# Optimization experiments

Hardware: AMD Instinct MI355X
Metric: run time of the kernel (lower is better)

The kernel has to match this reference:

```python
import jax, jax.numpy as jnp
import numpy as np

B, LT, LI, DT, DI, D, H = 128, 96, 64, 1024, 2048, 1024, 4
NEG = -2.0 ** 31  # tf.pow(-2.0, 31)
EPS = 1e-3        # keras LayerNormalization default epsilon


def _mha(q_in, k_in, v_in, q_mask, k_mask, Wq, Wk, Wv, Wo):
    # tf split-heads: chunk i of axis 2 -> head i; reshape (B,L,H,d) matches.
    d = D // H
    b = q_in.shape[0]
    q = (q_in @ Wq).reshape(b, -1, H, d)
    k = (k_in @ Wk).reshape(b, -1, H, d)
    v = (v_in @ Wv).reshape(b, -1, H, d)
    scores = jnp.einsum('bqhd,bkhd->bhqk', q, k) / jnp.sqrt(jnp.float32(d))
    mask = (q_mask != 0)[:, None, :, None] & (k_mask != 0)[:, None, None, :]  # [B,1,Lq,Lk]
    scores = jnp.where(mask, scores, NEG)
    attn = jax.nn.softmax(scores, axis=-1)
    attn = jnp.where(mask, attn, 0.0)  # dropout rate is 0.0 -> identity
    out = jnp.einsum('bhqk,bkhd->bqhd', attn, v).reshape(b, -1, D)
    return out @ Wo


def _ln(x, g, b):
    m = jnp.mean(x, axis=-1, keepdims=True)
    v = jnp.var(x, axis=-1, keepdims=True)
    return (x - m) / jnp.sqrt(v + EPS) * g + b


def setup_inputs() -> dict:
    key = jax.random.key(0)
    ks = iter(jax.random.split(key, 40))
    s = 0.02
    inp = {
        'text_embedding': jax.random.normal(next(ks), (B, LT, DT), jnp.float32),
        'image_embedding': jax.random.normal(next(ks), (B, LI, DI), jnp.float32),
        'text_mask': jax.random.randint(next(ks), (B, LT), 0, 2, jnp.int32),
        'image_mask': jax.random.randint(next(ks), (B, LI), 0, 2, jnp.int32),
        'W_tp': jax.random.normal(next(ks), (DT, D), jnp.float32) * s,
        'b_tp': jnp.zeros((D,), jnp.float32),
        'W_ip': jax.random.normal(next(ks), (DI, D), jnp.float32) * s,
        'b_ip': jnp.zeros((D,), jnp.float32),
        # text cross-attn (query=image_proj, key=text_proj, value=RAW text)
        'ta_Wq': jax.random.normal(next(ks), (D, D), jnp.float32) * s,
        'ta_Wk': jax.random.normal(next(ks), (D, D), jnp.float32) * s,
        'ta_Wv': jax.random.normal(next(ks), (DT, D), jnp.float32) * s,
        'ta_Wo': jax.random.normal(next(ks), (D, D), jnp.float32) * s,
        # image cross-attn (query=text_proj, key=image_proj, value=RAW image)
        'ia_Wq': jax.random.normal(next(ks), (D, D), jnp.float32) * s,
        'ia_Wk': jax.random.normal(next(ks), (D, D), jnp.float32) * s,
        'ia_Wv': jax.random.normal(next(ks), (DI, D), jnp.float32) * s,
        'ia_Wo': jax.random.normal(next(ks), (D, D), jnp.float32) * s,
        # self-attention blocks
        'ts_Wq': jax.random.normal(next(ks), (D, D), jnp.float32) * s,
        'ts_Wk': jax.random.normal(next(ks), (D, D), jnp.float32) * s,
        'ts_Wv': jax.random.normal(next(ks), (D, D), jnp.float32) * s,
        'ts_Wo': jax.random.normal(next(ks), (D, D), jnp.float32) * s,
        'is_Wq': jax.random.normal(next(ks), (D, D), jnp.float32) * s,
        'is_Wk': jax.random.normal(next(ks), (D, D), jnp.float32) * s,
        'is_Wv': jax.random.normal(next(ks), (D, D), jnp.float32) * s,
        'is_Wo': jax.random.normal(next(ks), (D, D), jnp.float32) * s,
        # layernorm params
        'ln_ta_g': jnp.ones((D,), jnp.float32), 'ln_ta_b': jnp.zeros((D,), jnp.float32),
        'ln_ia_g': jnp.ones((D,), jnp.float32), 'ln_ia_b': jnp.zeros((D,), jnp.float32),
        'ln_ts_g': jnp.ones((D,), jnp.float32), 'ln_ts_b': jnp.zeros((D,), jnp.float32),
        'ln_is_g': jnp.ones((D,), jnp.float32), 'ln_is_b': jnp.zeros((D,), jnp.float32),
    }
    return inp


def reference(text_embedding, image_embedding, text_mask, image_mask,
              W_tp, b_tp, W_ip, b_ip,
              ta_Wq, ta_Wk, ta_Wv, ta_Wo,
              ia_Wq, ia_Wk, ia_Wv, ia_Wo,
              ts_Wq, ts_Wk, ts_Wv, ts_Wo,
              is_Wq, is_Wk, is_Wv, is_Wo,
              ln_ta_g, ln_ta_b, ln_ia_g, ln_ia_b,
              ln_ts_g, ln_ts_b, ln_is_g, ln_is_b):
    text_proj = text_embedding @ W_tp + b_tp    # [B,LT,D]
    image_proj = image_embedding @ W_ip + b_ip  # [B,LI,D]
    # cross attention (note asymmetric query/key masks, raw-value inputs)
    text_att = _mha(image_proj, text_proj, text_embedding, image_mask, text_mask,
                    ta_Wq, ta_Wk, ta_Wv, ta_Wo)   # [B,LI,D]
    image_att = _mha(text_proj, image_proj, image_embedding, text_mask, image_mask,
                     ia_Wq, ia_Wk, ia_Wv, ia_Wo)  # [B,LT,D]
    text_att = _ln(text_att, ln_ta_g, ln_ta_b)
    image_att = _ln(image_att, ln_ia_g, ln_ia_b)
    # self attention
    text_att = _mha(text_att, text_att, text_att, image_mask, image_mask,
                    ts_Wq, ts_Wk, ts_Wv, ts_Wo)
    image_att = _mha(image_att, image_att, image_att, text_mask, text_mask,
                     is_Wq, is_Wk, is_Wv, is_Wo)
    text_att = _ln(text_att, ln_ts_g, ln_ts_b)
    image_att = _ln(image_att, ln_is_g, ln_is_b)
    return (text_att, image_att)
```

## Files before the change

### kernel.cpp

```cpp
#include <hip/hip_runtime.h>

typedef __bf16 bf16_t;
typedef __attribute__((ext_vector_type(8))) __bf16 bf16x8;
typedef __attribute__((ext_vector_type(4))) __bf16 bf16x4;
typedef __attribute__((ext_vector_type(4))) float f32x4;

__device__ __forceinline__ void async_copy16(const bf16_t* g, bf16_t* l) {
    __builtin_amdgcn_global_load_lds(
        (const __attribute__((address_space(1))) void*)g,
        (__attribute__((address_space(3))) void*)l, 16, 0, 0);
}

__global__ __launch_bounds__(256) void cvt_bf16(const float* __restrict__ in,
                                                bf16_t* __restrict__ out) {
    int i = (blockIdx.x * 256 + threadIdx.x) * 4;
    float4 v = *(const float4*)(in + i);
    bf16x4 o;
    o[0] = (__bf16)v.x; o[1] = (__bf16)v.y; o[2] = (__bf16)v.z; o[3] = (__bf16)v.w;
    *(bf16x4*)(out + i) = o;
}

__global__ __launch_bounds__(256) void transpose_group(const float* __restrict__ s0,
                                                       const float* __restrict__ s1,
                                                       const float* __restrict__ s2,
                                                       bf16_t* __restrict__ dst, int K) {
    const float* in;
    if (blockIdx.z == 0) in = s0;
    else if (blockIdx.z == 1) in = s1;
    else in = s2;
    bf16_t* out = dst + (size_t)blockIdx.z * 1024 * K;
    __shared__ float tile[32][33];
    int t = threadIdx.x;
    int tx = t & 31, ty = t >> 5;
    int n0 = blockIdx.x * 32, k0 = blockIdx.y * 32;
#pragma unroll
    for (int i = 0; i < 4; i++) {
        int k = k0 + ty + i * 8;
        tile[ty + i * 8][tx] = in[(size_t)k * 1024 + n0 + tx];
    }
    __syncthreads();
#pragma unroll
    for (int i = 0; i < 4; i++) {
        int n = n0 + ty + i * 8;
        out[(size_t)n * K + k0 + tx] = (bf16_t)tile[tx][ty + i * 8];
    }
}

__global__ __launch_bounds__(256) void fuse_bias(const float* __restrict__ src,
                                                 float* __restrict__ out) {
    int i = blockIdx.x * 256 + threadIdx.x;
    out[i] = (i < 1024) ? src[i] : 0.f;
}

__global__ __launch_bounds__(256, 2) void gemm256(const bf16_t* __restrict__ A,
                                                  const bf16_t* __restrict__ Bt,
                                                  const float* __restrict__ bias,
                                                  bf16_t* __restrict__ o0,
                                                  bf16_t* __restrict__ o1,
                                                  bf16_t* __restrict__ o2,
                                                  int M, int N, int K) {
    (void)M; (void)N;
    __shared__ bf16_t Ls[36864];
    const int t = threadIdx.x;
    const int w = t >> 6, lane = t & 63;
    const int l16 = lane & 15, quad = lane >> 4;
    const int wm = (w >> 1) * 128, wn = (w & 1) * 64;

    const int nx = gridDim.x;
    const int nwg = nx * gridDim.y;
    const int flat = blockIdx.y * nx + blockIdx.x;
    const int chunk = nwg >> 3;
    const int swz = (flat & 7) * chunk + (flat >> 3);
    const int bm = (swz % nx) * 256;
    const int bn = (swz / nx) * 128;

    const int NT = K >> 5;

    const int sl = t & 7;
    const int pl8 = t >> 3;
    const int ss = sl ^ (pl8 & 7);
    const int srow = (pl8 << 1) | (ss >> 2);
    const int scol = (ss & 3) << 3;
    const bf16_t* pA = A + (size_t)(bm + srow) * K + scol;
    const bf16_t* pB = Bt + (size_t)(bn + srow) * K + scol;
    const int ldW = w * 512;

    auto stageA = [&](int tt, int bi) {
        bf16_t* d = Ls + bi * 8192 + ldW;
        const bf16_t* s = pA + (size_t)tt * 32;
        async_copy16(s, d);
        async_copy16(s + (size_t)64 * K, d + 2048);
        async_copy16(s + (size_t)128 * K, d + 4096);
        async_copy16(s + (size_t)192 * K, d + 6144);
    };
    auto stageB = [&](int tt, int bi) {
        bf16_t* d = Ls + 24576 + bi * 4096 + ldW;
        const bf16_t* s = pB + (size_t)tt * 32;
        async_copy16(s, d);
        async_copy16(s + (size_t)64 * K, d + 2048);
    };

    int offA[8], offB[4];
#pragma unroll
    for (int mf = 0; mf < 8; mf++) {
        int row = wm + mf * 16 + l16;
        int p = row >> 1;
        int s2 = (((row & 1) << 2) | quad) ^ (p & 7);
        offA[mf] = p * 64 + s2 * 8;
    }
#pragma unroll
    for (int nf = 0; nf < 4; nf++) {
        int row = wn + nf * 16 + l16;
        int p = row >> 1;
        int s2 = (((row & 1) << 2) | quad) ^ (p & 7);
        offB[nf] = p * 64 + s2 * 8;
    }

    const f32x4 zero = {0.f, 0.f, 0.f, 0.f};
    f32x4 acc[8][4];
#pragma unroll
    for (int i = 0; i < 8; i++)
#pragma unroll
        for (int j = 0; j < 4; j++) acc[i][j] = zero;

    stageA(0, 0); stageB(0, 0);
    stageA(1, 1); stageB(1, 1);
    asm volatile("s_waitcnt vmcnt(6)" ::: "memory");
    __builtin_amdgcn_s_barrier();
    __builtin_amdgcn_sched_barrier(0);

    int ri = 0;
    for (int t0 = 0; t0 < NT; ++t0) {
        const bf16_t* ca = Ls + ri * 8192;
        const bf16_t* cbv = Ls + 24576 + ri * 4096;
        const int si = (ri >= 1) ? ri - 1 : 2;
        const bool st2 = (t0 + 2 < NT);

        if (st2) stageA(t0 + 2, si);
        bf16x8 bq[4], aq[4], ar[4];
#pragma unroll
        for (int nf = 0; nf < 4; nf++) bq[nf] = *(const bf16x8*)(cbv + offB[nf]);
#pragma unroll
        for (int mf = 0; mf < 4; mf++) aq[mf] = *(const bf16x8*)(ca + offA[mf]);
        if (st2) stageB(t0 + 2, si);
        __builtin_amdgcn_s_barrier();
        __builtin_amdgcn_s_setprio(1);
#pragma unroll
        for (int mf = 0; mf < 4; mf++)
#pragma unroll
            for (int nf = 0; nf < 4; nf++)
                acc[mf][nf] = __builtin_amdgcn_mfma_f32_16x16x32_bf16(aq[mf], bq[nf], acc[mf][nf], 0, 0, 0);
        __builtin_amdgcn_s_setprio(0);
        __builtin_amdgcn_s_barrier();

#pragma unroll
        for (int mf = 0; mf < 4; mf++) ar[mf] = *(const bf16x8*)(ca + offA[4 + mf]);
        __builtin_amdgcn_s_barrier();
        __builtin_amdgcn_s_setprio(1);
#pragma unroll
        for (int mf = 0; mf < 4; mf++)
#pragma unroll
            for (int nf = 0; nf < 4; nf++)
                acc[4 + mf][nf] = __builtin_amdgcn_mfma_f32_16x16x32_bf16(ar[mf], bq[nf], acc[4 + mf][nf], 0, 0, 0);
        __builtin_amdgcn_s_setprio(0);

        if (t0 + 1 < NT) {
            if (st2) asm volatile("s_waitcnt vmcnt(6)" ::: "memory");
            else     asm volatile("s_waitcnt vmcnt(0)" ::: "memory");
            __builtin_amdgcn_s_barrier();
            __builtin_amdgcn_sched_barrier(0);
        }
        ri = (ri == 2) ? 0 : ri + 1;
    }

    bf16_t* outp;
    if (bn < 1024) outp = o0;
    else if (bn < 2048) outp = o1;
    else outp = o2;
    const int cseg = bn & 1023;
    float bsv[4];
#pragma unroll
    for (int nf = 0; nf < 4; nf++)
        bsv[nf] = bias ? bias[bn + wn + nf * 16 + l16] : 0.f;
#pragma unroll
    for (int mf = 0; mf < 8; mf++) {
        int r0 = bm + wm + mf * 16 + quad * 4;
#pragma unroll
        for (int nf = 0; nf < 4; nf++) {
            int c = cseg + wn + nf * 16 + l16;
#pragma unroll
            for (int r = 0; r < 4; r++)
                outp[(size_t)(r0 + r) * 1024 + c] = (bf16_t)(acc[mf][nf][r] + bsv[nf]);
        }
    }
}

template <int LQ, int LK>
__global__ __launch_bounds__(256) void attn_kernel(const bf16_t* __restrict__ Q,
                                                   const bf16_t* __restrict__ Kb,
                                                   const bf16_t* __restrict__ V,
                                                   const int* __restrict__ qmask,
                                                   const int* __restrict__ kmask,
                                                   bf16_t* __restrict__ O) {
    constexpr int VSTR = LK + 8;
    constexpr int NQT = LQ / 16, NKT = LK / 16, NKB = LK / 32;
    __shared__ bf16_t Vt[256 * VSTR];
    __shared__ bf16_t Pb[4 * 16 * LK];

    const int t = threadIdx.x;
    const int w = t >> 6, lane = t & 63;
    const int quad = lane >> 4, l16 = lane & 15;
    const int b = blockIdx.x >> 2;
    const int h = blockIdx.x & 3;
    const int hoff = h * 256;

    for (int idx = t; idx < LK * 32; idx += 256) {
        int k = idx % LK;
        int e0 = (idx / LK) * 8;
        bf16x8 v = *(const bf16x8*)(V + (size_t)(b * LK + k) * 1024 + hoff + e0);
#pragma unroll
        for (int j = 0; j < 8; j++) Vt[(e0 + j) * VSTR + k] = v[j];
    }
    __syncthreads();

    bf16_t* P = Pb + w * (16 * LK);

    for (int qt = w; qt < NQT; qt += 4) {
        const int qrow = b * LQ + qt * 16;
        bf16x8 qf[8];
#pragma unroll
        for (int kb = 0; kb < 8; kb++)
            qf[kb] = *(const bf16x8*)(Q + (size_t)(qrow + l16) * 1024 + hoff + kb * 32 + quad * 8);

        f32x4 s[NKT];
        const f32x4 zero = {0.f, 0.f, 0.f, 0.f};
#pragma unroll
        for (int nt = 0; nt < NKT; nt++) {
            f32x4 a = zero;
#pragma unroll
            for (int kb = 0; kb < 8; kb++) {
                bf16x8 kf = *(const bf16x8*)(Kb + (size_t)(b * LK + nt * 16 + l16) * 1024 + hoff + kb * 32 + quad * 8);
                a = __builtin_amdgcn_mfma_f32_16x16x32_bf16(qf[kb], kf, a, 0, 0, 0);
            }
            s[nt] = a;
        }

        int km[NKT];
#pragma unroll
        for (int nt = 0; nt < NKT; nt++) km[nt] = kmask[b * LK + nt * 16 + l16];
        int qmv[4];
#pragma unroll
        for (int r = 0; r < 4; r++) qmv[r] = qmask[b * LQ + qt * 16 + quad * 4 + r];

        float rmax[4], rsum[4];
#pragma unroll
        for (int r = 0; r < 4; r++) rmax[r] = -3.0e38f;
#pragma unroll
        for (int nt = 0; nt < NKT; nt++)
#pragma unroll
            for (int r = 0; r < 4; r++) {
                float v = s[nt][r] * 0.0625f;
                bool ok = (qmv[r] != 0) && (km[nt] != 0);
                s[nt][r] = ok ? v : -3.0e38f;
                rmax[r] = fmaxf(rmax[r], s[nt][r]);
            }
#pragma unroll
        for (int r = 0; r < 4; r++)
            for (int off = 1; off < 16; off <<= 1)
                rmax[r] = fmaxf(rmax[r], __shfl_xor(rmax[r], off, 16));
#pragma unroll
        for (int r = 0; r < 4; r++) rsum[r] = 0.f;
#pragma unroll
        for (int nt = 0; nt < NKT; nt++)
#pragma unroll
            for (int r = 0; r < 4; r++) {
                float p = (s[nt][r] > -1.0e38f) ? __expf(s[nt][r] - rmax[r]) : 0.f;
                s[nt][r] = p;
                rsum[r] += p;
            }
#pragma unroll
        for (int r = 0; r < 4; r++)
            for (int off = 1; off < 16; off <<= 1)
                rsum[r] += __shfl_xor(rsum[r], off, 16);
#pragma unroll
        for (int r = 0; r < 4; r++) rsum[r] = (rsum[r] > 0.f) ? 1.f / rsum[r] : 0.f;

#pragma unroll
        for (int nt = 0; nt < NKT; nt++)
#pragma unroll
            for (int r = 0; r < 4; r++)
                P[(quad * 4 + r) * LK + nt * 16 + l16] = (bf16_t)(s[nt][r] * rsum[r]);
        asm volatile("s_waitcnt lgkmcnt(0)" ::: "memory");

        bf16x8 pf[NKB];
#pragma unroll
        for (int kb = 0; kb < NKB; kb++)
            pf[kb] = *(const bf16x8*)(P + l16 * LK + kb * 32 + quad * 8);

#pragma unroll
        for (int et = 0; et < 16; et++) {
            f32x4 o = zero;
#pragma unroll
            for (int kb = 0; kb < NKB; kb++) {
                bf16x8 vf = *(const bf16x8*)(Vt + (et * 16 + l16) * VSTR + kb * 32 + quad * 8);
                o = __builtin_amdgcn_mfma_f32_16x16x32_bf16(pf[kb], vf, o, 0, 0, 0);
            }
#pragma unroll
            for (int r = 0; r < 4; r++)
                O[(size_t)(qrow + quad * 4 + r) * 1024 + hoff + et * 16 + l16] = (bf16_t)o[r];
        }
    }
}

__global__ __launch_bounds__(256) void ln_kernel(const bf16_t* __restrict__ in,
                                                 const float* __restrict__ g,
                                                 const float* __restrict__ be,
                                                 float* __restrict__ outF,
                                                 bf16_t* __restrict__ outB) {
    __shared__ float red[8];
    const int row = blockIdx.x, t = threadIdx.x;
    bf16x4 xb = *(const bf16x4*)(in + (size_t)row * 1024 + t * 4);
    float x0 = (float)xb[0], x1 = (float)xb[1], x2 = (float)xb[2], x3 = (float)xb[3];
    float s = x0 + x1 + x2 + x3;
    float ss = x0 * x0 + x1 * x1 + x2 * x2 + x3 * x3;
    for (int off = 1; off < 64; off <<= 1) {
        s += __shfl_xor(s, off);
        ss += __shfl_xor(ss, off);
    }
    int w = t >> 6, lane = t & 63;
    if (lane == 0) { red[w * 2] = s; red[w * 2 + 1] = ss; }
    __syncthreads();
    if (t == 0) {
        float a = 0.f, b2 = 0.f;
        for (int i = 0; i < 4; i++) { a += red[i * 2]; b2 += red[i * 2 + 1]; }
        red[0] = a; red[1] = b2;
    }
    __syncthreads();
    float mean = red[0] * (1.f / 1024.f);
    float var = red[1] * (1.f / 1024.f) - mean * mean;
    float rstd = rsqrtf(var + 1e-3f);
    float4 gv = *(const float4*)(g + t * 4);
    float4 bv = *(const float4*)(be + t * 4);
    float y0 = (x0 - mean) * rstd * gv.x + bv.x;
    float y1 = (x1 - mean) * rstd * gv.y + bv.y;
    float y2 = (x2 - mean) * rstd * gv.z + bv.z;
    float y3 = (x3 - mean) * rstd * gv.w + bv.w;
    if (outF) {
        float4 o = {y0, y1, y2, y3};
        *(float4*)(outF + (size_t)row * 1024 + t * 4) = o;
    }
    if (outB) {
        bf16x4 o;
        o[0] = (__bf16)y0; o[1] = (__bf16)y1; o[2] = (__bf16)y2; o[3] = (__bf16)y3;
        *(bf16x4*)(outB + (size_t)row * 1024 + t * 4) = o;
    }
}

extern "C" void kernel_launch(void* const* d_in, const int* in_sizes, int n_in,
                              void* d_out, int out_size, void* d_ws, size_t ws_size,
                              hipStream_t stream) {
    (void)in_sizes; (void)n_in; (void)out_size; (void)ws_size;
    const float* tE = (const float*)d_in[0];
    const float* iE = (const float*)d_in[1];
    const int* tMask = (const int*)d_in[2];
    const int* iMask = (const int*)d_in[3];

    const size_t MB = 1048576;
    char* ws = (char*)d_ws;
    bf16_t* WB = (bf16_t*)ws;
    float* biasT = (float*)(ws + 8 * MB);
    float* biasI = biasT + 2048;
    char* AB = ws + 9 * MB;
    auto buf = [&](int mb) { return (bf16_t*)(AB + (size_t)mb * MB); };

    auto TG = [&](int i0, int i1, int i2, int parts, int K) {
        transpose_group<<<dim3(32, K / 32, parts), 256, 0, stream>>>(
            (const float*)d_in[i0], i1 >= 0 ? (const float*)d_in[i1] : (const float*)d_in[i0],
            i2 >= 0 ? (const float*)d_in[i2] : (const float*)d_in[i0], WB, K);
    };
    auto gemm = [&](const bf16_t* A, const float* bias, bf16_t* out0, bf16_t* out1,
                    bf16_t* out2, int M, int N, int K) {
        gemm256<<<dim3(M / 256, N / 128), 256, 0, stream>>>(A, WB, bias, out0, out1, out2, M, N, K);
    };

    fuse_bias<<<8, 256, 0, stream>>>((const float*)d_in[5], biasT);
    fuse_bias<<<8, 256, 0, stream>>>((const float*)d_in[7], biasI);

    cvt_bf16<<<12288, 256, 0, stream>>>(tE, buf(88));
    TG(4, 10, -1, 2, 1024);
    gemm(buf(88), biasT, buf(32), buf(64), nullptr, 12288, 2048, 1024);
    cvt_bf16<<<16384, 256, 0, stream>>>(iE, buf(88));
    TG(6, 14, -1, 2, 2048);
    gemm(buf(88), biasI, buf(0), buf(16), nullptr, 8192, 2048, 2048);
    TG(9, 12, -1, 2, 1024);
    gemm(buf(32), nullptr, buf(88), buf(112), nullptr, 12288, 2048, 1024);
    TG(8, 13, -1, 2, 1024);
    gemm(buf(0), nullptr, buf(32), buf(48), nullptr, 8192, 2048, 1024);
    attn_kernel<64, 96><<<512, 256, 0, stream>>>(buf(32), buf(88), buf(64), iMask, tMask, buf(0));
    attn_kernel<96, 64><<<512, 256, 0, stream>>>(buf(112), buf(48), buf(16), tMask, iMask, buf(64));
    TG(11, -1, -1, 1, 1024);
    gemm(buf(0), nullptr, buf(32), nullptr, nullptr, 8192, 1024, 1024);
    ln_kernel<<<8192, 256, 0, stream>>>(buf(32), (const float*)d_in[24], (const float*)d_in[25], nullptr, buf(88));
    TG(15, -1, -1, 1, 1024);
    gemm(buf(64), nullptr, buf(0), nullptr, nullptr, 12288, 1024, 1024);
    ln_kernel<<<12288, 256, 0, stream>>>(buf(0), (const float*)d_in[26], (const float*)d_in[27], nullptr, buf(104));
    TG(16, 17, 18, 3, 1024);
    gemm(buf(88), nullptr, buf(0), buf(16), buf(32), 8192, 3072, 1024);
    attn_kernel<64, 64><<<512, 256, 0, stream>>>(buf(0), buf(16), buf(32), iMask, iMask, buf(48));
    TG(19, -1, -1, 1, 1024);
    gemm(buf(48), nullptr, buf(64), nullptr, nullptr, 8192, 1024, 1024);
    ln_kernel<<<8192, 256, 0, stream>>>(buf(64), (const float*)d_in[28], (const float*)d_in[29], (float*)d_out, nullptr);
    TG(20, 21, 22, 3, 1024);
    gemm(buf(104), nullptr, buf(0), buf(24), buf(48), 12288, 3072, 1024);
    attn_kernel<96, 96><<<512, 256, 0, stream>>>(buf(0), buf(24), buf(48), tMask, tMask, buf(72));
    TG(23, -1, -1, 1, 1024);
    gemm(buf(72), nullptr, buf(96), nullptr, nullptr, 12288, 1024, 1024);
    ln_kernel<<<12288, 256, 0, stream>>>(buf(96), (const float*)d_in[30], (const float*)d_in[31],
                                         (float*)d_out + 8388608, nullptr);
}
```

Before: 1.003 ms.

## Make GEMM persistent with atomic tile tickets and load all A fragments at once

The GEMM kernel becomes persistent: at most 512 workgroups are launched, and each repeatedly claims the next output tile from a global atomic ticket counter, with one counter slot per GEMM call. The slots are zeroed by a memset at the start of the launch. The inner loop is also restructured to load all eight A fragments before one block of 32 MFMAs, which removes two intra-iteration barriers but raises register pressure. The intent is to cut tail effects and launch/scheduling overhead, at the cost of an atomic plus a __syncthreads per tile.

```diff
diff --git a/kernel.cpp b/kernel.cpp
--- a/kernel.cpp
+++ b/kernel.cpp
@@ -58,47 +58,24 @@
                                                   bf16_t* __restrict__ o0,
                                                   bf16_t* __restrict__ o1,
                                                   bf16_t* __restrict__ o2,
-                                                  int M, int N, int K) {
-    (void)M; (void)N;
+                                                  int K, int nTx, int nTiles,
+                                                  unsigned* __restrict__ ticket) {
     __shared__ bf16_t Ls[36864];
+    __shared__ int sF;
     const int t = threadIdx.x;
     const int w = t >> 6, lane = t & 63;
     const int l16 = lane & 15, quad = lane >> 4;
     const int wm = (w >> 1) * 128, wn = (w & 1) * 64;
 
-    const int nx = gridDim.x;
-    const int nwg = nx * gridDim.y;
-    const int flat = blockIdx.y * nx + blockIdx.x;
-    const int chunk = nwg >> 3;
-    const int swz = (flat & 7) * chunk + (flat >> 3);
-    const int bm = (swz % nx) * 256;
-    const int bn = (swz / nx) * 128;
-
     const int NT = K >> 5;
+    const int chunk = nTiles >> 3;
 
     const int sl = t & 7;
     const int pl8 = t >> 3;
     const int ss = sl ^ (pl8 & 7);
     const int srow = (pl8 << 1) | (ss >> 2);
     const int scol = (ss & 3) << 3;
-    const bf16_t* pA = A + (size_t)(bm + srow) * K + scol;
-    const bf16_t* pB = Bt + (size_t)(bn + srow) * K + scol;
     const int ldW = w * 512;
-
-    auto stageA = [&](int tt, int bi) {
-        bf16_t* d = Ls + bi * 8192 + ldW;
-        const bf16_t* s = pA + (size_t)tt * 32;
-        async_copy16(s, d);
-        async_copy16(s + (size_t)64 * K, d + 2048);
-        async_copy16(s + (size_t)128 * K, d + 4096);
-        async_copy16(s + (size_t)192 * K, d + 6144);
-    };
-    auto stageB = [&](int tt, int bi) {
-        bf16_t* d = Ls + 24576 + bi * 4096 + ldW;
-        const bf16_t* s = pB + (size_t)tt * 32;
-        async_copy16(s, d);
-        async_copy16(s + (size_t)64 * K, d + 2048);
-    };
 
     int offA[8], offB[4];
 #pragma unroll
@@ -117,80 +94,104 @@
     }
 
     const f32x4 zero = {0.f, 0.f, 0.f, 0.f};
-    f32x4 acc[8][4];
-#pragma unroll
-    for (int i = 0; i < 8; i++)
-#pragma unroll
-        for (int j = 0; j < 4; j++) acc[i][j] = zero;
-
-    stageA(0, 0); stageB(0, 0);
-    stageA(1, 1); stageB(1, 1);
-    asm volatile("s_waitcnt vmcnt(6)" ::: "memory");
-    __builtin_amdgcn_s_barrier();
-    __builtin_amdgcn_sched_barrier(0);
-
-    int ri = 0;
-    for (int t0 = 0; t0 < NT; ++t0) {
-        const bf16_t* ca = Ls + ri * 8192;
-        const bf16_t* cbv = Ls + 24576 + ri * 4096;
-        const int si = (ri >= 1) ? ri - 1 : 2;
-        const bool st2 = (t0 + 2 < NT);
-
-        if (st2) stageA(t0 + 2, si);
-        bf16x8 bq[4], aq[4], ar[4];
-#pragma unroll
-        for (int nf = 0; nf < 4; nf++) bq[nf] = *(const bf16x8*)(cbv + offB[nf]);
-#pragma unroll
-        for (int mf = 0; mf < 4; mf++) aq[mf] = *(const bf16x8*)(ca + offA[mf]);
-        if (st2) stageB(t0 + 2, si);
+
+    for (;;) {
+        if (t == 0) sF = (int)atomicAdd(ticket, 1u);
+        __syncthreads();
+        const int flat = sF;
+        if (flat >= nTiles) return;
+        const int swz = (flat & 7) * chunk + (flat >> 3);
+        const int bm = (swz % nTx) * 256;
+        const int bn = (swz / nTx) * 128;
+
+        const bf16_t* pA = A + (size_t)(bm + srow) * K + scol;
+        const bf16_t* pB = Bt + (size_t)(bn + srow) * K + scol;
+
+        f32x4 acc[8][4];
+#pragma unroll
+        for (int i = 0; i < 8; i++)
+#pragma unroll
+            for (int j = 0; j < 4; j++) acc[i][j] = zero;
+
+#pragma unroll
+        for (int pt = 0; pt < 2; pt++) {
+            bf16_t* da = Ls + pt * 8192 + ldW;
+            const bf16_t* sa = pA + (size_t)pt * 32;
+            async_copy16(sa, da);
+            async_copy16(sa + (size_t)64 * K, da + 2048);
+            async_copy16(sa + (size_t)128 * K, da + 4096);
+            async_copy16(sa + (size_t)192 * K, da + 6144);
+            bf16_t* db = Ls + 24576 + pt * 4096 + ldW;
+            const bf16_t* sb = pB + (size_t)pt * 32;
+            async_copy16(sb, db);
+            async_copy16(sb + (size_t)64 * K, db + 2048);
+        }
+        asm volatile("s_waitcnt vmcnt(6)" ::: "memory");
         __builtin_amdgcn_s_barrier();
-        __builtin_amdgcn_s_setprio(1);
-#pragma unroll
-        for (int mf = 0; mf < 4; mf++)
-#pragma unroll
-            for (int nf = 0; nf < 4; nf++)
-                acc[mf][nf] = __builtin_amdgcn_mfma_f32_16x16x32_bf16(aq[mf], bq[nf], acc[mf][nf], 0, 0, 0);
-        __builtin_amdgcn_s_setprio(0);
-        __builtin_amdgcn_s_barrier();
-
-#pragma unroll
-        for (int mf = 0; mf < 4; mf++) ar[mf] = *(const bf16x8*)(ca + offA[4 + mf]);
-        __builtin_amdgcn_s_barrier();
-        __builtin_amdgcn_s_setprio(1);
-#pragma unroll
-        for (int mf = 0; mf < 4; mf++)
-#pragma unroll
-            for (int nf = 0; nf < 4; nf++)
-                acc[4 + mf][nf] = __builtin_amdgcn_mfma_f32_16x16x32_bf16(ar[mf], bq[nf], acc[4 + mf][nf], 0, 0, 0);
-        __builtin_amdgcn_s_setprio(0);
-
-        if (t0 + 1 < NT) {
-            if (st2) asm volatile("s_waitcnt vmcnt(6)" ::: "memory");
-            else     asm volatile("s_waitcnt vmcnt(0)" ::: "memory");
-            __builtin_amdgcn_s_barrier();
-            __builtin_amdgcn_sched_barrier(0);
+        __builtin_amdgcn_sched_barrier(0);
+
+        int ri = 0;
+        for (int t0 = 0; t0 < NT; ++t0) {
+            const bf16_t* ca = Ls + ri * 8192;
+            const bf16_t* cbv = Ls + 24576 + ri * 4096;
+            const int si = (ri >= 1) ? ri - 1 : 2;
+            const bool st2 = (t0 + 2 < NT);
+
+            if (st2) {
+                bf16_t* d = Ls + si * 8192 + ldW;
+                const bf16_t* s = pA + (size_t)(t0 + 2) * 32;
+                async_copy16(s, d);
+                async_copy16(s + (size_t)64 * K, d + 2048);
+                async_copy16(s + (size_t)128 * K, d + 4096);
+                async_copy16(s + (size_t)192 * K, d + 6144);
+            }
+            bf16x8 bq[4], aq[8];
+#pragma unroll
+            for (int nf = 0; nf < 4; nf++) bq[nf] = *(const bf16x8*)(cbv + offB[nf]);
+#pragma unroll
+            for (int mf = 0; mf < 8; mf++) aq[mf] = *(const bf16x8*)(ca + offA[mf]);
+            if (st2) {
+                bf16_t* d = Ls + 24576 + si * 4096 + ldW;
+                const bf16_t* s = pB + (size_t)(t0 + 2) * 32;
+                async_copy16(s, d);
+                async_copy16(s + (size_t)64 * K, d + 2048);
+            }
+            __builtin_amdgcn_s_setprio(1);
+#pragma unroll
+            for (int mf = 0; mf < 8; mf++)
+#pragma unroll
+                for (int nf = 0; nf < 4; nf++)
+                    acc[mf][nf] = __builtin_amdgcn_mfma_f32_16x16x32_bf16(aq[mf], bq[nf], acc[mf][nf], 0, 0, 0);
+            __builtin_amdgcn_s_setprio(0);
+
+            if (t0 + 1 < NT) {
+                if (st2) asm volatile("s_waitcnt vmcnt(6)" ::: "memory");
+                else     asm volatile("s_waitcnt vmcnt(0)" ::: "memory");
+                __builtin_amdgcn_s_barrier();
+                __builtin_amdgcn_sched_barrier(0);
+            }
+            ri = (ri == 2) ? 0 : ri + 1;
         }
-        ri = (ri == 2) ? 0 : ri + 1;
-    }
-
-    bf16_t* outp;
-    if (bn < 1024) outp = o0;
-    else if (bn < 2048) outp = o1;
-    else outp = o2;
-    const int cseg = bn & 1023;
-    float bsv[4];
-#pragma unroll
-    for (int nf = 0; nf < 4; nf++)
-        bsv[nf] = bias ? bias[bn + wn + nf * 16 + l16] : 0.f;
-#pragma unroll
-    for (int mf = 0; mf < 8; mf++) {
-        int r0 = bm + wm + mf * 16 + quad * 4;
-#pragma unroll
-        for (int nf = 0; nf < 4; nf++) {
-            int c = cseg + wn + nf * 16 + l16;
-#pragma unroll
-            for (int r = 0; r < 4; r++)
-                outp[(size_t)(r0 + r) * 1024 + c] = (bf16_t)(acc[mf][nf][r] + bsv[nf]);
+
+        bf16_t* outp;
+        if (bn < 1024) outp = o0;
+        else if (bn < 2048) outp = o1;
+        else outp = o2;
+        const int cseg = bn & 1023;
+        float bsv[4];
+#pragma unroll
+        for (int nf = 0; nf < 4; nf++)
+            bsv[nf] = bias ? bias[bn + wn + nf * 16 + l16] : 0.f;
+#pragma unroll
+        for (int mf = 0; mf < 8; mf++) {
+            int r0 = bm + wm + mf * 16 + quad * 4;
+#pragma unroll
+            for (int nf = 0; nf < 4; nf++) {
+                int c = cseg + wn + nf * 16 + l16;
+#pragma unroll
+                for (int r = 0; r < 4; r++)
+                    outp[(size_t)(r0 + r) * 1024 + c] = (bf16_t)(acc[mf][nf][r] + bsv[nf]);
+            }
         }
     }
 }
@@ -370,17 +371,24 @@
     bf16_t* WB = (bf16_t*)ws;
     float* biasT = (float*)(ws + 8 * MB);
     float* biasI = biasT + 2048;
+    unsigned* tickets = (unsigned*)(ws + 8 * MB + 65536);
     char* AB = ws + 9 * MB;
     auto buf = [&](int mb) { return (bf16_t*)(AB + (size_t)mb * MB); };
+
+    hipMemsetAsync(tickets, 0, 64, stream);
 
     auto TG = [&](int i0, int i1, int i2, int parts, int K) {
         transpose_group<<<dim3(32, K / 32, parts), 256, 0, stream>>>(
             (const float*)d_in[i0], i1 >= 0 ? (const float*)d_in[i1] : (const float*)d_in[i0],
             i2 >= 0 ? (const float*)d_in[i2] : (const float*)d_in[i0], WB, K);
     };
+    int slot = 0;
     auto gemm = [&](const bf16_t* A, const float* bias, bf16_t* out0, bf16_t* out1,
                     bf16_t* out2, int M, int N, int K) {
-        gemm256<<<dim3(M / 256, N / 128), 256, 0, stream>>>(A, WB, bias, out0, out1, out2, M, N, K);
+        int nTx = M / 256, nT = nTx * (N / 128);
+        int grid = nT < 512 ? nT : 512;
+        gemm256<<<grid, 256, 0, stream>>>(A, WB, bias, out0, out1, out2, K, nTx, nT, tickets + slot);
+        slot++;
     };
 
     fuse_bias<<<8, 256, 0, stream>>>((const float*)d_in[5], biasT);
```

New measurement: 1.041 ms. 3.8% more time.
